# Performance work log

Hardware: AMD Instinct MI355X
Metric: run time of the kernel (lower is better)

## Reference

```python
import jax, jax.numpy as jnp
import numpy as np

FS = 3152
NFFT = 512
NPERSEG = 512
NOVERLAP = 341
STEP = NPERSEG - NOVERLAP  # 171
F_UP = 1500
F_LOW = 1


def _a_weight_linear(freqs):
    """10**(A(f)/10) with A(0) -> 0 weight (A(0) = -inf in the torch code)."""
    f1, f2, f3, f4 = 20.6, 107.7, 737.9, 12194.0
    A1000 = -2.0
    fsq = freqs ** 2
    num = (f4 ** 2) * freqs ** 4
    den = (fsq + f1 ** 2) * jnp.sqrt(fsq + f2 ** 2) * jnp.sqrt(fsq + f3 ** 2) * (fsq + f4 ** 2)
    A = 20.0 * jnp.log10(num / den) - A1000
    return jnp.where(freqs > 0, 10.0 ** (A / 10.0), 0.0)


def setup_inputs() -> dict:
    key = jax.random.key(0)
    x = jax.random.normal(key, (64, 262144), dtype=jnp.float32)
    return {"x": x}


def reference(x):
    B, T = x.shape
    nseg = (T - NPERSEG) // STEP + 1
    # Batched unfold via gather: [B, nseg, NPERSEG]
    idx = np.arange(nseg)[:, None] * STEP + np.arange(NPERSEG)[None, :]
    # periodic Hamming window (torch.hamming_window(periodic=True))
    window = (0.54 - 0.46 * jnp.cos(2.0 * jnp.pi * jnp.arange(NPERSEG) / NPERSEG)).astype(x.dtype)
    segs = x[:, idx] * window  # [B, nseg, 512]
    spec = jnp.fft.rfft(segs, n=NFFT, axis=-1)  # [B, nseg, 257]
    win_power = jnp.sum(window ** 2)
    psd = (spec.real ** 2 + spec.imag ** 2) / (win_power * FS)
    # one-sided correction: double all bins except DC and Nyquist
    scale = jnp.ones(NFFT // 2 + 1, dtype=x.dtype).at[1:-1].set(2.0)
    pxx = (psd * scale).mean(axis=1)  # [B, 257]

    freqs = jnp.arange(NFFT // 2 + 1, dtype=jnp.float32) * (FS / NFFT)
    aw = _a_weight_linear(freqs)  # [257]

    f_res = FS / NFFT
    lo = int(np.floor(F_LOW / f_res + 1)) - 1  # = 0
    hi = int(np.floor(F_UP / f_res + 1))       # = 244
    # 10**((10*log10(pxx)+A)/10) == pxx * 10**(A/10)
    band = jnp.sum(pxx[:, lo:hi] * aw[lo:hi], axis=1)  # [B]
    level_A = 10.0 * jnp.log10(band)
    return jnp.sum(level_A) / B
```

## Files before the change

kernel.cpp:

```cpp
#include <hip/hip_runtime.h>
#include <math.h>

#ifndef M_PI
#define M_PI 3.14159265358979323846
#endif

#define T_LEN   262144
#define NBATCH  64
#define STEP    171
#define NSEG    1531
#define NPAIR   766
#define WPB     128
#define HI_BIN  244

__device__ __forceinline__ int bitrev3(int r) {
    return ((r & 1) << 2) | (r & 2) | ((r & 4) >> 2);
}

__device__ __forceinline__ void pswap32(float& a, float& b) {
    asm volatile("v_permlane32_swap_b32 %0, %1" : "+v"(a), "+v"(b));
}
__device__ __forceinline__ void pswap16(float& a, float& b) {
    asm volatile("v_permlane16_swap_b32 %0, %1" : "+v"(a), "+v"(b));
}
template <int CTRL>
__device__ __forceinline__ float dppq(float x) {
    return __int_as_float(__builtin_amdgcn_mov_dpp(__float_as_int(x), CTRL, 0xF, 0xF, true));
}
template <int OFF>
__device__ __forceinline__ float swz(float x) {
    return __int_as_float(__builtin_amdgcn_ds_swizzle(__float_as_int(x), OFF));
}

__global__ __launch_bounds__(256) void fft_band_k(const float* __restrict__ x,
                                                  float* __restrict__ ws) {
    const int lane   = threadIdx.x & 63;
    const int waveId = (int)(blockIdx.x * 256 + threadIdx.x) >> 6;
    const int b      = waveId >> 7;
    const int winb   = waveId & (WPB - 1);
    const int L = lane;

    float wv[8];
#pragma unroll
    for (int r = 0; r < 8; ++r) {
        float n = (float)(L + 64 * r);
        wv[r] = 0.54f - 0.46f * __cosf((float)(2.0 * M_PI / 512.0) * n);
    }
    float wt[8];
#pragma unroll
    for (int p = 0; p < 8; ++p) {
        int k = 4 * ((L >> 5) & 1) + 2 * ((L >> 4) & 1) + ((p >> 2) & 1)
              + 8 * ((p & 1) + 2 * ((p >> 1) & 1) + 4 * ((L >> 3) & 1)
                     + 8 * ((L >> 2) & 1) + 16 * ((L >> 1) & 1) + 32 * (L & 1));
        int mb = (k <= 256) ? k : 512 - k;
        float wgt = 0.0f;
        if (mb >= 1 && mb < HI_BIN) {
            float f   = (float)mb * (3152.0f / 512.0f);
            float fsq = f * f;
            float num = 1.48693636e8f * fsq * fsq;
            float d1  = fsq + 424.36f;
            float d2  = fsq + 11599.29f;
            float d3  = fsq + 544496.41f;
            float d4  = fsq + 1.48693636e8f;
            float ratio = (num / (d1 * d4)) * rsqrtf(d2 * d3);
            wgt = ratio * ratio * 1.6141422e-9f;
        }
        wt[p] = wgt;
    }
    float mre[8], mim[8];
#pragma unroll
    for (int r = 0; r < 8; ++r) {
        float ang = (float)(-2.0 * M_PI / 512.0) * (float)(bitrev3(r) * L);
        float s, c; __sincosf(ang, &s, &c);
        mre[r] = c; mim[r] = s;
    }
    float c32, s32, c16, s16;
    __sincosf((float)(-2.0 * M_PI) * (float)(L & 31) / 64.0f, &s32, &c32);
    __sincosf((float)(-2.0 * M_PI) * (float)(L & 15) / 32.0f, &s16, &c16);
    float c8, s8, g8, c4, s4, g4, c2, s2, g2, g1;
    if (L & 8) { __sincosf((float)(-2.0 * M_PI) * (float)(L & 7) / 16.0f, &s8, &c8); g8 = -1.0f; }
    else       { c8 = 1.0f; s8 = 0.0f; g8 = 1.0f; }
    if (L & 4) { __sincosf((float)(-2.0 * M_PI) * (float)(L & 3) / 8.0f, &s4, &c4); g4 = -1.0f; }
    else       { c4 = 1.0f; s4 = 0.0f; g4 = 1.0f; }
    if (L & 2) { c2 = (L & 1) ? 0.0f : 1.0f; s2 = (L & 1) ? -1.0f : 0.0f; g2 = -1.0f; }
    else       { c2 = 1.0f; s2 = 0.0f; g2 = 1.0f; }
    g1 = (L & 1) ? -1.0f : 1.0f;

    const float C707 = 0.70710678118654752f;
    float acc = 0.0f;
    const float* xb = x + (size_t)b * T_LEN;

    for (int p = winb; p < NPAIR; p += WPB) {
        const int s0 = 2 * p, s1 = 2 * p + 1;
        float zre[8], zim[8];
        const float* p0 = xb + s0 * STEP + L;
#pragma unroll
        for (int r = 0; r < 8; ++r) zre[r] = p0[64 * r] * wv[r];
        if (s1 < NSEG) {
            const float* p1 = xb + s1 * STEP + L;
#pragma unroll
            for (int r = 0; r < 8; ++r) zim[r] = p1[64 * r] * wv[r];
        } else {
#pragma unroll
            for (int r = 0; r < 8; ++r) zim[r] = 0.0f;
        }

        float tre, tim;
        tre = zre[0] - zre[4]; tim = zim[0] - zim[4];
        zre[0] += zre[4]; zim[0] += zim[4];
        zre[4] = tre; zim[4] = tim;
        tre = zre[1] - zre[5]; tim = zim[1] - zim[5];
        zre[1] += zre[5]; zim[1] += zim[5];
        zre[5] = C707 * (tre + tim); zim[5] = C707 * (tim - tre);
        tre = zre[2] - zre[6]; tim = zim[2] - zim[6];
        zre[2] += zre[6]; zim[2] += zim[6];
        zre[6] = tim; zim[6] = -tre;
        tre = zre[3] - zre[7]; tim = zim[3] - zim[7];
        zre[3] += zre[7]; zim[3] += zim[7];
        zre[7] = C707 * (tim - tre); zim[7] = -C707 * (tre + tim);
        tre = zre[0] - zre[2]; tim = zim[0] - zim[2];
        zre[0] += zre[2]; zim[0] += zim[2];
        zre[2] = tre; zim[2] = tim;
        tre = zre[1] - zre[3]; tim = zim[1] - zim[3];
        zre[1] += zre[3]; zim[1] += zim[3];
        zre[3] = tim; zim[3] = -tre;
        tre = zre[4] - zre[6]; tim = zim[4] - zim[6];
        zre[4] += zre[6]; zim[4] += zim[6];
        zre[6] = tre; zim[6] = tim;
        tre = zre[5] - zre[7]; tim = zim[5] - zim[7];
        zre[5] += zre[7]; zim[5] += zim[7];
        zre[7] = tim; zim[7] = -tre;
#pragma unroll
        for (int g = 0; g < 8; g += 2) {
            tre = zre[g] - zre[g + 1]; tim = zim[g] - zim[g + 1];
            zre[g] += zre[g + 1]; zim[g] += zim[g + 1];
            zre[g + 1] = tre; zim[g + 1] = tim;
        }

#pragma unroll
        for (int r = 1; r < 8; ++r) {
            float a = zre[r] * mre[r] - zim[r] * mim[r];
            zim[r] = zre[r] * mim[r] + zim[r] * mre[r];
            zre[r] = a;
        }

#pragma unroll
        for (int q = 0; q < 8; q += 2) {
            pswap32(zre[q], zre[q + 1]);
            pswap32(zim[q], zim[q + 1]);
            float sr = zre[q] + zre[q + 1], si = zim[q] + zim[q + 1];
            float dr = zre[q] - zre[q + 1], di = zim[q] - zim[q + 1];
            zre[q] = sr; zim[q] = si;
            zre[q + 1] = dr * c32 - di * s32;
            zim[q + 1] = dr * s32 + di * c32;
        }
        {
            const int qs[4] = {0, 1, 4, 5};
#pragma unroll
            for (int t = 0; t < 4; ++t) {
                const int q = qs[t];
                pswap16(zre[q], zre[q + 2]);
                pswap16(zim[q], zim[q + 2]);
                float sr = zre[q] + zre[q + 2], si = zim[q] + zim[q + 2];
                float dr = zre[q] - zre[q + 2], di = zim[q] - zim[q + 2];
                zre[q] = sr; zim[q] = si;
                zre[q + 2] = dr * c16 - di * s16;
                zim[q + 2] = dr * s16 + di * c16;
            }
        }
#pragma unroll
        for (int q = 0; q < 8; ++q) {
            float pr = swz<0x201F>(zre[q]), pi = swz<0x201F>(zim[q]);
            float nr = fmaf(g8, zre[q], pr), ni = fmaf(g8, zim[q], pi);
            zre[q] = nr * c8 - ni * s8; zim[q] = nr * s8 + ni * c8;
        }
#pragma unroll
        for (int q = 0; q < 8; ++q) {
            float pr = swz<0x101F>(zre[q]), pi = swz<0x101F>(zim[q]);
            float nr = fmaf(g4, zre[q], pr), ni = fmaf(g4, zim[q], pi);
            zre[q] = nr * c4 - ni * s4; zim[q] = nr * s4 + ni * c4;
        }
#pragma unroll
        for (int q = 0; q < 8; ++q) {
            float pr = dppq<0x4E>(zre[q]), pi = dppq<0x4E>(zim[q]);
            float nr = fmaf(g2, zre[q], pr), ni = fmaf(g2, zim[q], pi);
            zre[q] = nr * c2 - ni * s2; zim[q] = nr * s2 + ni * c2;
        }
#pragma unroll
        for (int q = 0; q < 8; ++q) {
            float pr = dppq<0xB1>(zre[q]), pi = dppq<0xB1>(zim[q]);
            float nr = fmaf(g1, zre[q], pr), ni = fmaf(g1, zim[q], pi);
            acc = fmaf(wt[q], fmaf(nr, nr, ni * ni), acc);
        }
    }

#pragma unroll
    for (int off = 32; off >= 1; off >>= 1) acc += __shfl_xor(acc, off, 64);
    if (lane == 0) ws[waveId] = acc;
}

__global__ void finalize_k(const float* __restrict__ ws, float* __restrict__ out) {
    __shared__ float red[256];
    int t = threadIdx.x;
    int b = t & 63, g = t >> 6;
    float s = 0.0f;
    for (int i = 0; i < 32; ++i) s += ws[b * 128 + g * 32 + i];
    red[t] = s;
    __syncthreads();
    if (t < 64) {
        float band = red[t] + red[t + 64] + red[t + 128] + red[t + 192];
        float lv = 10.0f * log10f(band);
#pragma unroll
        for (int off = 32; off >= 1; off >>= 1) lv += __shfl_xor(lv, off, 64);
        if (t == 0) out[0] = lv * (1.0f / 64.0f);
    }
}

extern "C" void kernel_launch(void* const* d_in, const int* in_sizes, int n_in,
                              void* d_out, int out_size, void* d_ws, size_t ws_size,
                              hipStream_t stream) {
    const float* x = (const float*)d_in[0];
    float* out = (float*)d_out;
    float* ws  = (float*)d_ws;
    fft_band_k<<<(NBATCH * WPB) / 4, 256, 0, stream>>>(x, ws);
    finalize_k<<<1, 256, 0, stream>>>(ws, out);
}
```

Before: 118.1 us.

## Pack complex FFT math into v_pk ops and fuse finalize via last-block atomics

Rewrites the per-wave radix FFT to keep complex values as float2 and do twiddle multiplies with packed v_pk_mul/v_pk_fma inline asm, with register pinning and launch_bounds occupancy hints. It also replaces one swizzle stage with a DPP row op. The separate finalize kernel is removed: partial sums are atomically added per batch and a last-block counter triggers the log10 reduction. A hipMemsetAsync is added to zero the workspace. The aim is fewer VALU instructions and one fewer kernel launch, at the cost of float atomics (nondeterministic sum order) and an extra memset.

```diff
diff --git a/kernel.cpp b/kernel.cpp
--- a/kernel.cpp
+++ b/kernel.cpp
@@ -13,6 +13,8 @@
 #define WPB     128
 #define HI_BIN  244
 
+typedef float v2f __attribute__((ext_vector_type(2)));
+
 __device__ __forceinline__ int bitrev3(int r) {
     return ((r & 1) << 2) | (r & 2) | ((r & 4) >> 2);
 }
@@ -24,7 +26,7 @@
     asm volatile("v_permlane16_swap_b32 %0, %1" : "+v"(a), "+v"(b));
 }
 template <int CTRL>
-__device__ __forceinline__ float dppq(float x) {
+__device__ __forceinline__ float dppf(float x) {
     return __int_as_float(__builtin_amdgcn_mov_dpp(__float_as_int(x), CTRL, 0xF, 0xF, true));
 }
 template <int OFF>
@@ -32,21 +34,32 @@
     return __int_as_float(__builtin_amdgcn_ds_swizzle(__float_as_int(x), OFF));
 }
 
-__global__ __launch_bounds__(256) void fft_band_k(const float* __restrict__ x,
-                                                  float* __restrict__ ws) {
-    const int lane   = threadIdx.x & 63;
+__device__ __forceinline__ v2f cmul(v2f z, v2f w) {
+    v2f t, d;
+    asm("v_pk_mul_f32 %0, %1, %2 op_sel_hi:[1,0]"
+        : "=v"(t) : "v"(z), "v"(w));
+    asm("v_pk_fma_f32 %0, %1, %2, %3 op_sel:[1,1,0] op_sel_hi:[0,1,1] neg_lo:[1,0,0]"
+        : "=v"(d) : "v"(z), "v"(w), "v"(t));
+    return d;
+}
+
+#define PIN(x) asm("" : "+v"(x))
+
+__global__ __launch_bounds__(256, 4) void fft_band_k(const float* __restrict__ x,
+                                                     float* __restrict__ ws,
+                                                     float* __restrict__ out) {
+    const int L      = threadIdx.x & 63;
     const int waveId = (int)(blockIdx.x * 256 + threadIdx.x) >> 6;
     const int b      = waveId >> 7;
     const int winb   = waveId & (WPB - 1);
-    const int L = lane;
-
-    float wv[8];
+
+    float wv[8], wt[8];
 #pragma unroll
     for (int r = 0; r < 8; ++r) {
         float n = (float)(L + 64 * r);
         wv[r] = 0.54f - 0.46f * __cosf((float)(2.0 * M_PI / 512.0) * n);
-    }
-    float wt[8];
+        PIN(wv[r]);
+    }
 #pragma unroll
     for (int p = 0; p < 8; ++p) {
         int k = 4 * ((L >> 5) & 1) + 2 * ((L >> 4) & 1) + ((p >> 2) & 1)
@@ -66,153 +79,146 @@
             wgt = ratio * ratio * 1.6141422e-9f;
         }
         wt[p] = wgt;
-    }
-    float mre[8], mim[8];
-#pragma unroll
-    for (int r = 0; r < 8; ++r) {
+        PIN(wt[p]);
+    }
+    v2f M[8];
+#pragma unroll
+    for (int r = 1; r < 8; ++r) {
         float ang = (float)(-2.0 * M_PI / 512.0) * (float)(bitrev3(r) * L);
         float s, c; __sincosf(ang, &s, &c);
-        mre[r] = c; mim[r] = s;
+        M[r] = (v2f){c, s};
+        PIN(M[r]);
     }
     float c32, s32, c16, s16;
     __sincosf((float)(-2.0 * M_PI) * (float)(L & 31) / 64.0f, &s32, &c32);
     __sincosf((float)(-2.0 * M_PI) * (float)(L & 15) / 32.0f, &s16, &c16);
-    float c8, s8, g8, c4, s4, g4, c2, s2, g2, g1;
-    if (L & 8) { __sincosf((float)(-2.0 * M_PI) * (float)(L & 7) / 16.0f, &s8, &c8); g8 = -1.0f; }
-    else       { c8 = 1.0f; s8 = 0.0f; g8 = 1.0f; }
-    if (L & 4) { __sincosf((float)(-2.0 * M_PI) * (float)(L & 3) / 8.0f, &s4, &c4); g4 = -1.0f; }
-    else       { c4 = 1.0f; s4 = 0.0f; g4 = 1.0f; }
-    if (L & 2) { c2 = (L & 1) ? 0.0f : 1.0f; s2 = (L & 1) ? -1.0f : 0.0f; g2 = -1.0f; }
-    else       { c2 = 1.0f; s2 = 0.0f; g2 = 1.0f; }
-    g1 = (L & 1) ? -1.0f : 1.0f;
+    v2f W32 = (v2f){c32, s32}; PIN(W32);
+    v2f W16 = (v2f){c16, s16}; PIN(W16);
+    v2f W8, W4, W2, g8v, g4v, g2v, g1v;
+    if (L & 8) { float s, c; __sincosf((float)(-2.0 * M_PI) * (float)(L & 7) / 16.0f, &s, &c);
+                 W8 = (v2f){c, s}; g8v = (v2f){-1.0f, -1.0f}; }
+    else       { W8 = (v2f){1.0f, 0.0f}; g8v = (v2f){1.0f, 1.0f}; }
+    if (L & 4) { float s, c; __sincosf((float)(-2.0 * M_PI) * (float)(L & 3) / 8.0f, &s, &c);
+                 W4 = (v2f){c, s}; g4v = (v2f){-1.0f, -1.0f}; }
+    else       { W4 = (v2f){1.0f, 0.0f}; g4v = (v2f){1.0f, 1.0f}; }
+    if (L & 2) { W2 = (L & 1) ? (v2f){0.0f, -1.0f} : (v2f){1.0f, 0.0f};
+                 g2v = (v2f){-1.0f, -1.0f}; }
+    else       { W2 = (v2f){1.0f, 0.0f}; g2v = (v2f){1.0f, 1.0f}; }
+    g1v = (L & 1) ? (v2f){-1.0f, -1.0f} : (v2f){1.0f, 1.0f};
+    PIN(W8); PIN(W4); PIN(W2); PIN(g8v); PIN(g4v); PIN(g2v); PIN(g1v);
 
     const float C707 = 0.70710678118654752f;
+    v2f W81 = (v2f){C707, -C707};  PIN(W81);
+    v2f W83 = (v2f){-C707, -C707}; PIN(W83);
+    v2f WNI = (v2f){0.0f, -1.0f};  PIN(WNI);
+
     float acc = 0.0f;
     const float* xb = x + (size_t)b * T_LEN;
 
     for (int p = winb; p < NPAIR; p += WPB) {
-        const int s0 = 2 * p, s1 = 2 * p + 1;
-        float zre[8], zim[8];
+        const int s0 = 2 * p;
+        v2f z[8];
         const float* p0 = xb + s0 * STEP + L;
-#pragma unroll
-        for (int r = 0; r < 8; ++r) zre[r] = p0[64 * r] * wv[r];
-        if (s1 < NSEG) {
-            const float* p1 = xb + s1 * STEP + L;
-#pragma unroll
-            for (int r = 0; r < 8; ++r) zim[r] = p1[64 * r] * wv[r];
+        float a[8], bb[8];
+#pragma unroll
+        for (int r = 0; r < 8; ++r) a[r] = p0[64 * r];
+        if (2 * p + 1 < NSEG) {
+#pragma unroll
+            for (int r = 0; r < 8; ++r) bb[r] = p0[64 * r + STEP];
         } else {
 #pragma unroll
-            for (int r = 0; r < 8; ++r) zim[r] = 0.0f;
-        }
-
-        float tre, tim;
-        tre = zre[0] - zre[4]; tim = zim[0] - zim[4];
-        zre[0] += zre[4]; zim[0] += zim[4];
-        zre[4] = tre; zim[4] = tim;
-        tre = zre[1] - zre[5]; tim = zim[1] - zim[5];
-        zre[1] += zre[5]; zim[1] += zim[5];
-        zre[5] = C707 * (tre + tim); zim[5] = C707 * (tim - tre);
-        tre = zre[2] - zre[6]; tim = zim[2] - zim[6];
-        zre[2] += zre[6]; zim[2] += zim[6];
-        zre[6] = tim; zim[6] = -tre;
-        tre = zre[3] - zre[7]; tim = zim[3] - zim[7];
-        zre[3] += zre[7]; zim[3] += zim[7];
-        zre[7] = C707 * (tim - tre); zim[7] = -C707 * (tre + tim);
-        tre = zre[0] - zre[2]; tim = zim[0] - zim[2];
-        zre[0] += zre[2]; zim[0] += zim[2];
-        zre[2] = tre; zim[2] = tim;
-        tre = zre[1] - zre[3]; tim = zim[1] - zim[3];
-        zre[1] += zre[3]; zim[1] += zim[3];
-        zre[3] = tim; zim[3] = -tre;
-        tre = zre[4] - zre[6]; tim = zim[4] - zim[6];
-        zre[4] += zre[6]; zim[4] += zim[6];
-        zre[6] = tre; zim[6] = tim;
-        tre = zre[5] - zre[7]; tim = zim[5] - zim[7];
-        zre[5] += zre[7]; zim[5] += zim[7];
-        zre[7] = tim; zim[7] = -tre;
-#pragma unroll
-        for (int g = 0; g < 8; g += 2) {
-            tre = zre[g] - zre[g + 1]; tim = zim[g] - zim[g + 1];
-            zre[g] += zre[g + 1]; zim[g] += zim[g + 1];
-            zre[g + 1] = tre; zim[g + 1] = tim;
-        }
-
-#pragma unroll
-        for (int r = 1; r < 8; ++r) {
-            float a = zre[r] * mre[r] - zim[r] * mim[r];
-            zim[r] = zre[r] * mim[r] + zim[r] * mre[r];
-            zre[r] = a;
-        }
+            for (int r = 0; r < 8; ++r) bb[r] = 0.0f;
+        }
+#pragma unroll
+        for (int r = 0; r < 8; ++r) z[r] = (v2f){a[r] * wv[r], bb[r] * wv[r]};
+
+        {
+            v2f d0 = z[0] - z[4]; z[0] += z[4];
+            v2f d1 = z[1] - z[5]; z[1] += z[5];
+            v2f d2 = z[2] - z[6]; z[2] += z[6];
+            v2f d3 = z[3] - z[7]; z[3] += z[7];
+            z[4] = d0;
+            z[5] = cmul(d1, W81);
+            z[6] = cmul(d2, WNI);
+            z[7] = cmul(d3, W83);
+            v2f t;
+            t = z[0] - z[2]; z[0] += z[2]; z[2] = t;
+            t = z[1] - z[3]; z[1] += z[3]; z[3] = cmul(t, WNI);
+            t = z[4] - z[6]; z[4] += z[6]; z[6] = t;
+            t = z[5] - z[7]; z[5] += z[7]; z[7] = cmul(t, WNI);
+#pragma unroll
+            for (int g = 0; g < 8; g += 2) {
+                t = z[g] - z[g + 1]; z[g] += z[g + 1]; z[g + 1] = t;
+            }
+        }
+
+#pragma unroll
+        for (int r = 1; r < 8; ++r) z[r] = cmul(z[r], M[r]);
 
 #pragma unroll
         for (int q = 0; q < 8; q += 2) {
-            pswap32(zre[q], zre[q + 1]);
-            pswap32(zim[q], zim[q + 1]);
-            float sr = zre[q] + zre[q + 1], si = zim[q] + zim[q + 1];
-            float dr = zre[q] - zre[q + 1], di = zim[q] - zim[q + 1];
-            zre[q] = sr; zim[q] = si;
-            zre[q + 1] = dr * c32 - di * s32;
-            zim[q + 1] = dr * s32 + di * c32;
+            float a0 = z[q].x, a1 = z[q].y, b0 = z[q + 1].x, b1 = z[q + 1].y;
+            pswap32(a0, b0); pswap32(a1, b1);
+            v2f A = (v2f){a0, a1}, B = (v2f){b0, b1};
+            v2f s = A + B, d = A - B;
+            z[q] = s; z[q + 1] = cmul(d, W32);
         }
         {
             const int qs[4] = {0, 1, 4, 5};
 #pragma unroll
-            for (int t = 0; t < 4; ++t) {
-                const int q = qs[t];
-                pswap16(zre[q], zre[q + 2]);
-                pswap16(zim[q], zim[q + 2]);
-                float sr = zre[q] + zre[q + 2], si = zim[q] + zim[q + 2];
-                float dr = zre[q] - zre[q + 2], di = zim[q] - zim[q + 2];
-                zre[q] = sr; zim[q] = si;
-                zre[q + 2] = dr * c16 - di * s16;
-                zim[q + 2] = dr * s16 + di * c16;
+            for (int t2 = 0; t2 < 4; ++t2) {
+                const int q = qs[t2];
+                float a0 = z[q].x, a1 = z[q].y, b0 = z[q + 2].x, b1 = z[q + 2].y;
+                pswap16(a0, b0); pswap16(a1, b1);
+                v2f A = (v2f){a0, a1}, B = (v2f){b0, b1};
+                v2f s = A + B, d = A - B;
+                z[q] = s; z[q + 2] = cmul(d, W16);
             }
         }
 #pragma unroll
         for (int q = 0; q < 8; ++q) {
-            float pr = swz<0x201F>(zre[q]), pi = swz<0x201F>(zim[q]);
-            float nr = fmaf(g8, zre[q], pr), ni = fmaf(g8, zim[q], pi);
-            zre[q] = nr * c8 - ni * s8; zim[q] = nr * s8 + ni * c8;
-        }
-#pragma unroll
-        for (int q = 0; q < 8; ++q) {
-            float pr = swz<0x101F>(zre[q]), pi = swz<0x101F>(zim[q]);
-            float nr = fmaf(g4, zre[q], pr), ni = fmaf(g4, zim[q], pi);
-            zre[q] = nr * c4 - ni * s4; zim[q] = nr * s4 + ni * c4;
-        }
-#pragma unroll
-        for (int q = 0; q < 8; ++q) {
-            float pr = dppq<0x4E>(zre[q]), pi = dppq<0x4E>(zim[q]);
-            float nr = fmaf(g2, zre[q], pr), ni = fmaf(g2, zim[q], pi);
-            zre[q] = nr * c2 - ni * s2; zim[q] = nr * s2 + ni * c2;
-        }
-#pragma unroll
-        for (int q = 0; q < 8; ++q) {
-            float pr = dppq<0xB1>(zre[q]), pi = dppq<0xB1>(zim[q]);
-            float nr = fmaf(g1, zre[q], pr), ni = fmaf(g1, zim[q], pi);
-            acc = fmaf(wt[q], fmaf(nr, nr, ni * ni), acc);
+            v2f pp = (v2f){dppf<0x128>(z[q].x), dppf<0x128>(z[q].y)};
+            v2f n = g8v * z[q] + pp;
+            z[q] = cmul(n, W8);
+        }
+#pragma unroll
+        for (int q = 0; q < 8; ++q) {
+            v2f pp = (v2f){swz<0x101F>(z[q].x), swz<0x101F>(z[q].y)};
+            v2f n = g4v * z[q] + pp;
+            z[q] = cmul(n, W4);
+        }
+#pragma unroll
+        for (int q = 0; q < 8; ++q) {
+            v2f pp = (v2f){dppf<0x4E>(z[q].x), dppf<0x4E>(z[q].y)};
+            v2f n = g2v * z[q] + pp;
+            z[q] = cmul(n, W2);
+        }
+#pragma unroll
+        for (int q = 0; q < 8; ++q) {
+            v2f pp = (v2f){dppf<0xB1>(z[q].x), dppf<0xB1>(z[q].y)};
+            v2f n = g1v * z[q] + pp;
+            acc = fmaf(wt[q], fmaf(n.x, n.x, n.y * n.y), acc);
         }
     }
 
 #pragma unroll
     for (int off = 32; off >= 1; off >>= 1) acc += __shfl_xor(acc, off, 64);
-    if (lane == 0) ws[waveId] = acc;
-}
-
-__global__ void finalize_k(const float* __restrict__ ws, float* __restrict__ out) {
-    __shared__ float red[256];
-    int t = threadIdx.x;
-    int b = t & 63, g = t >> 6;
-    float s = 0.0f;
-    for (int i = 0; i < 32; ++i) s += ws[b * 128 + g * 32 + i];
-    red[t] = s;
+    if (L == 0) atomicAdd(&ws[b], acc);
+
+    __shared__ int lastFlag;
     __syncthreads();
-    if (t < 64) {
-        float band = red[t] + red[t + 64] + red[t + 128] + red[t + 192];
+    if (threadIdx.x == 0) {
+        __threadfence();
+        unsigned old = atomicAdd((unsigned int*)(ws + 64), 1u);
+        lastFlag = (old == (unsigned)(gridDim.x - 1));
+    }
+    __syncthreads();
+    if (lastFlag && threadIdx.x < 64) {
+        float band = atomicAdd(&ws[threadIdx.x], 0.0f);
         float lv = 10.0f * log10f(band);
 #pragma unroll
         for (int off = 32; off >= 1; off >>= 1) lv += __shfl_xor(lv, off, 64);
-        if (t == 0) out[0] = lv * (1.0f / 64.0f);
+        if (threadIdx.x == 0) out[0] = lv * (1.0f / 64.0f);
     }
 }
 
@@ -222,6 +228,6 @@
     const float* x = (const float*)d_in[0];
     float* out = (float*)d_out;
     float* ws  = (float*)d_ws;
-    fft_band_k<<<(NBATCH * WPB) / 4, 256, 0, stream>>>(x, ws);
-    finalize_k<<<1, 256, 0, stream>>>(ws, out);
-}
+    hipMemsetAsync(ws, 0, 65 * sizeof(float), stream);
+    fft_band_k<<<(NBATCH * WPB) / 4, 256, 0, stream>>>(x, ws, out);
+}
```

After: 187.4 us. 1.59x slower.
